# Kernel optimization log

Measured on AMD Instinct MI355X. Metric: run time of the kernel, lower is better.

Reference implementation:

```python
import jax, jax.numpy as jnp
import numpy as np

B, T, C = 2, 2048, 1024
H, HS = 16, 64
THETA = 10000.0


def _rope_tables(seq_len, dim, dtype):
    inv_freq = 1.0 / (THETA ** (jnp.arange(0, dim, 2, dtype=jnp.float32) / dim))
    t = jnp.arange(seq_len, dtype=jnp.float32)
    freqs = t[:, None] * inv_freq[None, :]          # [T, dim/2]
    emb = jnp.concatenate([freqs, freqs], axis=-1)  # [T, dim]
    return jnp.cos(emb).astype(dtype), jnp.sin(emb).astype(dtype)


def _rotate_half(x):
    x1, x2 = jnp.split(x, 2, axis=-1)
    return jnp.concatenate([-x2, x1], axis=-1)


def setup_inputs() -> dict:
    key = jax.random.key(0)
    ks = jax.random.split(key, 9)
    s = 0.02
    return {
        "q_x": jax.random.normal(ks[0], (B, T, C), dtype=jnp.float32),
        "wq": jax.random.normal(ks[1], (C, H * HS), dtype=jnp.float32) * s,
        "bq": jnp.zeros((H * HS,), dtype=jnp.float32),
        "wk": jax.random.normal(ks[2], (C, H * HS), dtype=jnp.float32) * s,
        "bk": jnp.zeros((H * HS,), dtype=jnp.float32),
        "wv": jax.random.normal(ks[3], (C, H * HS), dtype=jnp.float32) * s,
        "bv": jnp.zeros((H * HS,), dtype=jnp.float32),
        "wc": jax.random.normal(ks[4], (H * HS, C), dtype=jnp.float32) * s,
        "bc": jnp.zeros((C,), dtype=jnp.float32),
    }


def reference(q_x, wq, bq, wk, bk, wv, bv, wc, bc):
    b, t, _ = q_x.shape
    # Q/K/V projections -> [B, H, T, HS]
    q = (q_x @ wq + bq).reshape(b, t, H, HS).transpose(0, 2, 1, 3)
    k = (q_x @ wk + bk).reshape(b, t, H, HS).transpose(0, 2, 1, 3)
    v = (q_x @ wv + bv).reshape(b, t, H, HS).transpose(0, 2, 1, 3)
    # RoPE (concat-half rotation)
    cos, sin = _rope_tables(t, HS, q.dtype)  # [T, HS]
    q = q * cos + _rotate_half(q) * sin
    k = k * cos + _rotate_half(k) * sin
    # Naive causal attention
    scale = 1.0 / np.sqrt(HS)
    att = jnp.einsum("bhqd,bhkd->bhqk", q, k) * scale
    mask = jnp.tril(jnp.ones((t, t), dtype=bool))
    att = jnp.where(mask, att, -jnp.inf)
    att = jax.nn.softmax(att, axis=-1)
    y = jnp.einsum("bhqk,bhkd->bhqd", att, v)
    y = y.transpose(0, 2, 1, 3).reshape(b, t, H * HS)
    return y @ wc + bc
```

## Files before the change

### kernel.cpp

```cpp
#include <hip/hip_runtime.h>

#define B_  2
#define T_  2048
#define C_  1024
#define H_  16
#define HS_ 64
#define M_  4096
#define N_  1024
#define K_  1024

typedef float floatx4 __attribute__((ext_vector_type(4)));
typedef short bf16x8  __attribute__((ext_vector_type(8)));

__device__ __forceinline__ float bf2f(unsigned short u) {
    return __uint_as_float(((unsigned int)u) << 16);
}
__device__ __forceinline__ unsigned short f2bf(float f) {
    unsigned int u = __float_as_uint(f);
    return (unsigned short)((u + 0x7fffu + ((u >> 16) & 1u)) >> 16);
}
__device__ __forceinline__ unsigned int pack2(float a, float b) {
    return (unsigned int)f2bf(a) | ((unsigned int)f2bf(b) << 16);
}
__device__ __forceinline__ unsigned int pack2t(float a, float b) {
    return __builtin_amdgcn_perm(__float_as_uint(b), __float_as_uint(a), 0x07060302u);
}
__device__ __forceinline__ void async16(const unsigned short* g, unsigned short* l) {
    __builtin_amdgcn_global_load_lds(
        (const __attribute__((address_space(1))) unsigned int*)g,
        (__attribute__((address_space(3))) unsigned int*)l, 16, 0, 0);
}

__global__ __launch_bounds__(256) void prep_kernel(
    const float* __restrict__ x,
    const float* __restrict__ w0, const float* __restrict__ w1,
    const float* __restrict__ w2, const float* __restrict__ w3,
    unsigned short* __restrict__ xb, unsigned short* __restrict__ wTall)
{
    __shared__ float tile[64][65];
    const int bid = blockIdx.x;
    const int t = threadIdx.x;
    if (bid < 4096) {
        const size_t i = ((size_t)bid * 256 + t) * 4;
        const float4 v = *(const float4*)(x + i);
        ushort4 st;
        st.x = f2bf(v.x); st.y = f2bf(v.y); st.z = f2bf(v.z); st.w = f2bf(v.w);
        *(ushort4*)(xb + i) = st;
        return;
    }
    const int zb = bid - 4096;
    const int z = zb >> 8, rem = zb & 255;
    const float* w = (z == 0) ? w0 : (z == 1) ? w1 : (z == 2) ? w2 : w3;
    unsigned short* wT = wTall + ((size_t)z << 20);
    const int n0 = (rem & 15) * 64, k0 = (rem >> 4) * 64;

    const int r = t >> 2, cq = (t & 3) * 16;
    const float4* src = (const float4*)(w + (size_t)(k0 + r) * N_ + n0 + cq);
    const float4 v0 = src[0], v1 = src[1], v2 = src[2], v3 = src[3];
    tile[r][cq+0]=v0.x; tile[r][cq+1]=v0.y; tile[r][cq+2]=v0.z; tile[r][cq+3]=v0.w;
    tile[r][cq+4]=v1.x; tile[r][cq+5]=v1.y; tile[r][cq+6]=v1.z; tile[r][cq+7]=v1.w;
    tile[r][cq+8]=v2.x; tile[r][cq+9]=v2.y; tile[r][cq+10]=v2.z; tile[r][cq+11]=v2.w;
    tile[r][cq+12]=v3.x; tile[r][cq+13]=v3.y; tile[r][cq+14]=v3.z; tile[r][cq+15]=v3.w;
    __syncthreads();

    const int rn = t >> 2, ck = (t & 3) * 16;
    unsigned int o[8];
#pragma unroll
    for (int ii = 0; ii < 8; ii++)
        o[ii] = pack2(tile[ck + 2*ii][rn], tile[ck + 2*ii + 1][rn]);
    unsigned short* dst = wT + (size_t)(n0 + rn) * K_ + k0 + ck;
    *(uint4*)dst       = make_uint4(o[0], o[1], o[2], o[3]);
    *(uint4*)(dst + 8) = make_uint4(o[4], o[5], o[6], o[7]);
}

__global__ __launch_bounds__(512, 2) void qkv_gemm(
    const unsigned short* __restrict__ xb, const unsigned short* __restrict__ wT,
    const float* __restrict__ bq, const float* __restrict__ bk,
    const float* __restrict__ bv,
    unsigned short* __restrict__ qb, unsigned short* __restrict__ kb,
    unsigned short* __restrict__ vb)
{
    __shared__ unsigned short lds[65536];

    const int tid  = threadIdx.x;
    const int lane = tid & 63;
    const int wave = tid >> 6;

    const int bid = blockIdx.x;
    const int swz = (bid & 7) * 24 + (bid >> 3);
    const int nb  = swz % 12;
    const int mb  = swz / 12;
    const int m0  = mb * 256;
    const int n0g = nb * 256;

    const int wm = wave >> 2, wn = wave & 3;
    const int fr = lane & 15, quad = lane >> 4;

    const int r_s = tid >> 2;
    const int c_s = (tid & 3) ^ ((tid >> 3) & 3);
    const unsigned short* aS0 = xb + (size_t)(m0 + r_s) * 1024 + c_s * 8;
    const unsigned short* aS1 = aS0 + (size_t)128 * 1024;
    const unsigned short* bS0 = wT + (size_t)(n0g + r_s) * 1024 + c_s * 8;
    const unsigned short* bS1 = bS0 + (size_t)128 * 1024;
    unsigned short* ldw = &lds[wave * 512];

    auto stage = [&](int buf, int region, const unsigned short* s0,
                     const unsigned short* s1) {
        unsigned short* d = ldw + buf * 32768 + region * 8192;
        async16(s0, d);
        async16(s1, d + 4096);
    };

    int oA[8], oB[4];
#pragma unroll
    for (int i = 0; i < 8; i++) {
        const int r = wm * 128 + i * 16 + fr;
        oA[i] = r * 32 + ((quad ^ ((r >> 1) & 3)) << 3);
    }
#pragma unroll
    for (int j = 0; j < 4; j++) {
        const int r = wn * 64 + j * 16 + fr;
        oB[j] = r * 32 + ((quad ^ ((r >> 1) & 3)) << 3);
    }

    floatx4 acc[8][4];
#pragma unroll
    for (int i = 0; i < 8; i++)
#pragma unroll
        for (int j = 0; j < 4; j++) acc[i][j] = (floatx4){0.f, 0.f, 0.f, 0.f};

    stage(0, 0, aS0,      aS1);
    stage(0, 2, bS0,      bS1);
    stage(0, 1, aS0 + 32, aS1 + 32);
    stage(0, 3, bS0 + 32, bS1 + 32);
    stage(1, 0, aS0 + 64, aS1 + 64);
    stage(1, 2, bS0 + 64, bS1 + 64);
    asm volatile("s_waitcnt vmcnt(8)" ::: "memory");
    __builtin_amdgcn_s_barrier();
    __builtin_amdgcn_sched_barrier(0);

    bf16x8 af[4], bfr[4];
#pragma unroll 2
    for (int t = 0; t < 16; ++t) {
        const int cur = t & 1, nxt = cur ^ 1;
        const unsigned short* A0 = &lds[cur * 32768];
        const unsigned short* A1 = A0 + 8192;
        const unsigned short* B0 = A0 + 16384;
        const unsigned short* B1 = A0 + 24576;
        const int k1 = (t + 1) * 64, k2 = (t + 2) * 64;

#pragma unroll
        for (int i = 0; i < 4; i++) af[i]  = *(const bf16x8*)&A0[oA[i]];
#pragma unroll
        for (int j = 0; j < 4; j++) bfr[j] = *(const bf16x8*)&B0[oB[j]];
        if (t + 1 < 16) stage(nxt, 1, aS0 + k1 + 32, aS1 + k1 + 32);
        __builtin_amdgcn_s_barrier();
        asm volatile("s_waitcnt lgkmcnt(0)" ::: "memory");
        __builtin_amdgcn_s_setprio(1);
#pragma unroll
        for (int i = 0; i < 4; i++)
#pragma unroll
            for (int j = 0; j < 4; j++)
                acc[i][j] = __builtin_amdgcn_mfma_f32_16x16x32_bf16(
                    af[i], bfr[j], acc[i][j], 0, 0, 0);
        __builtin_amdgcn_s_setprio(0);
        __builtin_amdgcn_s_barrier();
        __builtin_amdgcn_sched_barrier(0);

#pragma unroll
        for (int i = 0; i < 4; i++) af[i] = *(const bf16x8*)&A0[oA[4 + i]];
        if (t + 1 < 16) stage(nxt, 3, bS0 + k1 + 32, bS1 + k1 + 32);
        asm volatile("s_waitcnt vmcnt(8)" ::: "memory");
        __builtin_amdgcn_s_barrier();
        asm volatile("s_waitcnt lgkmcnt(0)" ::: "memory");
        __builtin_amdgcn_s_setprio(1);
#pragma unroll
        for (int i = 0; i < 4; i++)
#pragma unroll
            for (int j = 0; j < 4; j++)
                acc[4 + i][j] = __builtin_amdgcn_mfma_f32_16x16x32_bf16(
                    af[i], bfr[j], acc[4 + i][j], 0, 0, 0);
        __builtin_amdgcn_s_setprio(0);
        __builtin_amdgcn_s_barrier();
        __builtin_amdgcn_sched_barrier(0);

#pragma unroll
        for (int i = 0; i < 4; i++) af[i]  = *(const bf16x8*)&A1[oA[i]];
#pragma unroll
        for (int j = 0; j < 4; j++) bfr[j] = *(const bf16x8*)&B1[oB[j]];
        if (t + 2 < 16) stage(cur, 0, aS0 + k2, aS1 + k2);
        __builtin_amdgcn_s_barrier();
        asm volatile("s_waitcnt lgkmcnt(0)" ::: "memory");
        __builtin_amdgcn_s_setprio(1);
#pragma unroll
        for (int i = 0; i < 4; i++)
#pragma unroll
            for (int j = 0; j < 4; j++)
                acc[i][j] = __builtin_amdgcn_mfma_f32_16x16x32_bf16(
                    af[i], bfr[j], acc[i][j], 0, 0, 0);
        __builtin_amdgcn_s_setprio(0);
        __builtin_amdgcn_s_barrier();
        __builtin_amdgcn_sched_barrier(0);

#pragma unroll
        for (int i = 0; i < 4; i++) af[i] = *(const bf16x8*)&A1[oA[4 + i]];
        if (t + 2 < 16) stage(cur, 2, bS0 + k2, bS1 + k2);
        asm volatile("s_waitcnt vmcnt(8)" ::: "memory");
        __builtin_amdgcn_s_barrier();
        asm volatile("s_waitcnt lgkmcnt(0)" ::: "memory");
        __builtin_amdgcn_s_setprio(1);
#pragma unroll
        for (int i = 0; i < 4; i++)
#pragma unroll
            for (int j = 0; j < 4; j++)
                acc[4 + i][j] = __builtin_amdgcn_mfma_f32_16x16x32_bf16(
                    af[i], bfr[j], acc[4 + i][j], 0, 0, 0);
        __builtin_amdgcn_s_setprio(0);
        __builtin_amdgcn_s_barrier();
        __builtin_amdgcn_sched_barrier(0);
    }

    const int p = nb >> 2;
    const int colbase = (nb & 3) * 256 + wn * 64;
    const int h = colbase >> 6;
    const int rb = quad * 4;
    const float* bias = (p == 0) ? bq : (p == 1) ? bk : bv;

    if (p == 2) {
#pragma unroll
        for (int j = 0; j < 4; j++) {
            const int d = j * 16 + fr;
            const float bz = bias[colbase + d];
#pragma unroll
            for (int i = 0; i < 8; i++) {
                const int row0 = m0 + wm * 128 + i * 16 + rb;
                const int bb = row0 >> 11, tt = row0 & 2047;
                ushort4 st;
                st.x = f2bf(acc[i][j][0] + bz);
                st.y = f2bf(acc[i][j][1] + bz);
                st.z = f2bf(acc[i][j][2] + bz);
                st.w = f2bf(acc[i][j][3] + bz);
                *(ushort4*)&vb[((size_t)(bb * H_ + h) * HS_ + d) * T_ + tt] = st;
            }
        }
    } else {
        unsigned short* out = (p == 0) ? qb : kb;
        const float qsc = (p == 0) ? 0.18033688011111772f : 1.0f;
        const float bz0 = bias[colbase + fr];
        const float bz1 = bias[colbase + 16 + fr];
        const float bz2 = bias[colbase + 32 + fr];
        const float bz3 = bias[colbase + 48 + fr];
        const float nl = -0.41524101186279297f;
        const float if0 = exp2f((float)fr * nl);
        const float if1 = exp2f((float)(fr + 16) * nl);
#pragma unroll
        for (int i = 0; i < 8; i++) {
#pragma unroll
            for (int pr = 0; pr < 4; pr++) {
                const int row = m0 + wm * 128 + i * 16 + rb + pr;
                const int bb = row >> 11, tt = row & 2047;
                float s0, c0, s1, c1;
                __sincosf((float)tt * if0, &s0, &c0);
                __sincosf((float)tt * if1, &s1, &c1);
                const float v0 = acc[i][0][pr] + bz0;
                const float v1 = acc[i][1][pr] + bz1;
                const float v2 = acc[i][2][pr] + bz2;
                const float v3 = acc[i][3][pr] + bz3;
                unsigned short* ob = out + ((size_t)(bb * H_ + h) * T_ + tt) * HS_ + fr;
                ob[0]  = f2bf((v0 * c0 - v2 * s0) * qsc);
                ob[16] = f2bf((v1 * c1 - v3 * s1) * qsc);
                ob[32] = f2bf((v2 * c0 + v0 * s0) * qsc);
                ob[48] = f2bf((v3 * c1 + v1 * s1) * qsc);
            }
        }
    }
}

__global__ __launch_bounds__(256) void attn_kernel(
    const unsigned short* __restrict__ qb, const unsigned short* __restrict__ kb,
    const unsigned short* __restrict__ vt, unsigned short* __restrict__ yb,
    unsigned short* __restrict__ Opart, float* __restrict__ Mpart)
{
    __shared__ unsigned short Ks[2][64 * 64];
    __shared__ unsigned short Vs[2][64 * 64];
    __shared__ unsigned short Ps[4][16 * 64];

    const int bh = blockIdx.x;
    const int b = bh >> 4, h = bh & 15;
    const int s = 47 - (int)blockIdx.y;
    int qt, ktlo, kthi, half;
    bool split;
    if (s < 16) { qt = s; ktlo = 0; kthi = qt; half = 0; split = false; }
    else {
        const int idx = s - 16;
        qt = 16 + (idx >> 1); half = idx & 1;
        const int nf = (qt + 2) >> 1;
        ktlo = half ? nf : 0;
        kthi = half ? qt : nf - 1;
        split = true;
    }
    const int r0 = qt * 64;
    const int tid  = threadIdx.x;
    const int lane = tid & 63;
    const int wave = tid >> 6;
    const int l4   = lane & 15;
    const int quad = lane >> 4;

    const int qrow_g = r0 + wave * 16 + l4;

    bf16x8 qf[2];
    {
        const unsigned short* qp = qb + ((size_t)bh * T_ + qrow_g) * HS_ + quad * 8;
        qf[0] = *(const bf16x8*)(qp);
        qf[1] = *(const bf16x8*)(qp + 32);
    }

    floatx4 o[4];
#pragma unroll
    for (int g = 0; g < 4; g++) o[g] = (floatx4){0.f, 0.f, 0.f, 0.f};
    float m = -1e30f, l = 0.f;

    const int srow = tid >> 2;
    const int sc16 = (tid & 3) * 16;
    const int ssw  = (srow & 7) * 8;
    const int psw  = (l4 & 7) * 8;

    const unsigned short* kp = kb + ((size_t)bh * T_ + srow) * HS_ + sc16;
    const unsigned short* vp = vt + ((size_t)(bh * 64 + srow)) * T_ + sc16;

    uint4 rk0 = *(const uint4*)(kp + (size_t)ktlo * 64 * HS_);
    uint4 rk1 = *(const uint4*)(kp + (size_t)ktlo * 64 * HS_ + 8);
    uint4 rv0 = *(const uint4*)(vp + ktlo * 64);
    uint4 rv1 = *(const uint4*)(vp + ktlo * 64 + 8);
    *(uint4*)&Ks[0][srow * 64 + ( sc16      ^ ssw)] = rk0;
    *(uint4*)&Ks[0][srow * 64 + ((sc16 + 8) ^ ssw)] = rk1;
    *(uint4*)&Vs[0][srow * 64 + ( sc16      ^ ssw)] = rv0;
    *(uint4*)&Vs[0][srow * 64 + ((sc16 + 8) ^ ssw)] = rv1;

    for (int kt = ktlo; kt <= kthi; kt++) {
        const int cur = (kt - ktlo) & 1;
        if (kt < kthi) {
            const unsigned short* kpn = kp + (size_t)(kt + 1) * (64 * HS_);
            const unsigned short* vpn = vp + (kt + 1) * 64;
            rk0 = *(const uint4*)kpn;
            rk1 = *(const uint4*)(kpn + 8);
            rv0 = *(const uint4*)vpn;
            rv1 = *(const uint4*)(vpn + 8);
        }
        __syncthreads();

        floatx4 sf[4];
        __builtin_amdgcn_s_setprio(1);
#pragma unroll
        for (int mg = 0; mg < 4; mg++) {
            const int key = mg * 16 + l4;
            const int ksw = (key & 7) * 8;
            const bf16x8 a0 = *(const bf16x8*)&Ks[cur][key * 64 + ( (quad * 8)       ^ ksw)];
            const bf16x8 a1 = *(const bf16x8*)&Ks[cur][key * 64 + (((quad * 8) + 32) ^ ksw)];
            floatx4 z = (floatx4){0.f, 0.f, 0.f, 0.f};
            z = __builtin_amdgcn_mfma_f32_16x16x32_bf16(a0, qf[0], z, 0, 0, 0);
            z = __builtin_amdgcn_mfma_f32_16x16x32_bf16(a1, qf[1], z, 0, 0, 0);
            sf[mg] = z;
        }
        __builtin_amdgcn_s_setprio(0);

        if (kt == qt) {
#pragma unroll
            for (int mg = 0; mg < 4; mg++)
#pragma unroll
                for (int r = 0; r < 4; r++)
                    if (kt * 64 + 16 * mg + quad * 4 + r > qrow_g)
                        sf[mg][r] = -1e30f;
        }

        float mx[4];
#pragma unroll
        for (int mg = 0; mg < 4; mg++)
            mx[mg] = fmaxf(fmaxf(sf[mg][0], sf[mg][1]),
                           fmaxf(sf[mg][2], sf[mg][3]));
        float tm = fmaxf(fmaxf(mx[0], mx[1]), fmaxf(mx[2], mx[3]));

        if (!__all(tm <= m + 8.f)) {
            tm = fmaxf(tm, __shfl_xor(tm, 16));
            tm = fmaxf(tm, __shfl_xor(tm, 32));
            const float mnew  = fmaxf(m, tm);
            const float alpha = __builtin_amdgcn_exp2f(m - mnew);
            l *= alpha;
#pragma unroll
            for (int g = 0; g < 4; g++) o[g] = o[g] * alpha;
            m = mnew;
        }

        float p[4][4];
        float psg[4];
#pragma unroll
        for (int mg = 0; mg < 4; mg++) {
#pragma unroll
            for (int r = 0; r < 4; r++)
                p[mg][r] = __builtin_amdgcn_exp2f(sf[mg][r] - m);
            psg[mg] = (p[mg][0] + p[mg][1]) + (p[mg][2] + p[mg][3]);
        }
        l += (psg[0] + psg[1]) + (psg[2] + psg[3]);

#pragma unroll
        for (int mg = 0; mg < 4; mg++) {
            const int kb4 = 16 * mg + quad * 4;
            const int off = ((kb4 & ~7) ^ psw) | (kb4 & 7);
            uint2 w;
            w.x = pack2t(p[mg][0], p[mg][1]);
            w.y = pack2t(p[mg][2], p[mg][3]);
            *(uint2*)&Ps[wave][l4 * 64 + off] = w;
        }

        const bf16x8 pf0 = *(const bf16x8*)&Ps[wave][l4 * 64 + ( (quad * 8)       ^ psw)];
        const bf16x8 pf1 = *(const bf16x8*)&Ps[wave][l4 * 64 + (((quad * 8) + 32) ^ psw)];
        __builtin_amdgcn_s_setprio(1);
#pragma unroll
        for (int g = 0; g < 4; g++) {
            const int vd  = g * 16 + l4;
            const int vsw = (vd & 7) * 8;
            const bf16x8 va0 = *(const bf16x8*)&Vs[cur][vd * 64 + ( (quad * 8)       ^ vsw)];
            const bf16x8 va1 = *(const bf16x8*)&Vs[cur][vd * 64 + (((quad * 8) + 32) ^ vsw)];
            o[g] = __builtin_amdgcn_mfma_f32_16x16x32_bf16(va0, pf0, o[g], 0, 0, 0);
            o[g] = __builtin_amdgcn_mfma_f32_16x16x32_bf16(va1, pf1, o[g], 0, 0, 0);
        }
        __builtin_amdgcn_s_setprio(0);

        if (kt < kthi) {
            const int nxt = cur ^ 1;
            *(uint4*)&Ks[nxt][srow * 64 + ( sc16      ^ ssw)] = rk0;
            *(uint4*)&Ks[nxt][srow * 64 + ((sc16 + 8) ^ ssw)] = rk1;
            *(uint4*)&Vs[nxt][srow * 64 + ( sc16      ^ ssw)] = rv0;
            *(uint4*)&Vs[nxt][srow * 64 + ((sc16 + 8) ^ ssw)] = rv1;
        }
    }

    l += __shfl_xor(l, 16);
    l += __shfl_xor(l, 32);

    if (!split) {
        const float invl = 1.f / l;
        unsigned short* yrow = yb + ((size_t)(b * T_ + qrow_g) * H_ + h) * HS_;
#pragma unroll
        for (int g = 0; g < 4; g++) {
            ushort4 st;
            st.x = f2bf(o[g][0] * invl);
            st.y = f2bf(o[g][1] * invl);
            st.z = f2bf(o[g][2] * invl);
            st.w = f2bf(o[g][3] * invl);
            *(ushort4*)&yrow[16 * g + quad * 4] = st;
        }
    } else {
        const int u  = (bh * 16 + (qt - 16)) * 2 + half;
        const int rl = wave * 16 + l4;
        unsigned short* Op = Opart + (size_t)u * 4096 + rl * 64;
#pragma unroll
        for (int g = 0; g < 4; g++) {
            ushort4 st;
            st.x = f2bf(o[g][0]);
            st.y = f2bf(o[g][1]);
            st.z = f2bf(o[g][2]);
            st.w = f2bf(o[g][3]);
            *(ushort4*)&Op[16 * g + quad * 4] = st;
        }
        if (quad == 0) {
            float* ml = Mpart + (size_t)u * 128;
            ml[rl]      = m;
            ml[64 + rl] = l;
        }
    }
}

__global__ __launch_bounds__(256) void attn_combine(
    const unsigned short* __restrict__ Opart, const float* __restrict__ Mpart,
    unsigned short* __restrict__ yb)
{
    const int u  = blockIdx.x;
    const int bh = u >> 4, qt = 16 + (u & 15);
    const int b = bh >> 4, h = bh & 15;
    const int t = threadIdx.x;
    const int r = t >> 2, c = (t & 3) * 16;

    const float* ml1 = Mpart + (size_t)(u * 2) * 128;
    const float* ml2 = ml1 + 128;
    const float m1 = ml1[r], l1 = ml1[64 + r];
    const float m2 = ml2[r], l2 = ml2[64 + r];
    const float M  = fmaxf(m1, m2);
    const float w1 = __builtin_amdgcn_exp2f(m1 - M);
    const float w2 = __builtin_amdgcn_exp2f(m2 - M);
    const float inv = 1.f / (l1 * w1 + l2 * w2);
    const float a1 = w1 * inv, a2 = w2 * inv;

    const unsigned short* O1 = Opart + (size_t)(u * 2)     * 4096 + r * 64 + c;
    const unsigned short* O2 = Opart + (size_t)(u * 2 + 1) * 4096 + r * 64 + c;
    unsigned short* yrow = yb + ((size_t)(b * T_ + qt * 64 + r) * H_ + h) * HS_ + c;

#pragma unroll
    for (int j = 0; j < 2; j++) {
        const uint4 u1 = *(const uint4*)(O1 + 8 * j);
        const uint4 u2 = *(const uint4*)(O2 + 8 * j);
        const unsigned int a[4] = {u1.x, u1.y, u1.z, u1.w};
        const unsigned int d[4] = {u2.x, u2.y, u2.z, u2.w};
        unsigned int ov[4];
#pragma unroll
        for (int q = 0; q < 4; q++) {
            const float y0 = bf2f((unsigned short)(a[q] & 0xffff)) * a1
                           + bf2f((unsigned short)(d[q] & 0xffff)) * a2;
            const float y1 = bf2f((unsigned short)(a[q] >> 16)) * a1
                           + bf2f((unsigned short)(d[q] >> 16)) * a2;
            ov[q] = pack2(y0, y1);
        }
        *(uint4*)(yrow + 8 * j) = make_uint4(ov[0], ov[1], ov[2], ov[3]);
    }
}

__global__ __launch_bounds__(256) void out_gemm(
    const unsigned short* __restrict__ A, const unsigned short* __restrict__ wcT,
    const float* __restrict__ bias, float* __restrict__ out)
{
    __shared__ unsigned short As[2 * 64 * 32];
    __shared__ unsigned short Bs[2 * 128 * 32];

    const int tid  = threadIdx.x;
    const int lane = tid & 63;
    const int wave = tid >> 6;
    const int n0 = blockIdx.x * 128;
    const int m0 = blockIdx.y * 64;

    const int lrow = lane >> 2, lch = (lane & 3) * 8;
    const unsigned short* ag  = A   + (size_t)(m0 + wave * 16 + lrow) * K_ + lch;
    const unsigned short* bg0 = wcT + (size_t)(n0 + wave * 32 + lrow) * K_ + lch;
    const unsigned short* bg1 = bg0 + (size_t)16 * K_;
    unsigned short* lA0  = &As[(wave * 16) * 32];
    unsigned short* lA1  = lA0 + 2048;
    unsigned short* lB00 = &Bs[(wave * 32) * 32];
    unsigned short* lB01 = &Bs[(wave * 32 + 16) * 32];
    unsigned short* lB10 = lB00 + 4096;
    unsigned short* lB11 = lB01 + 4096;

    const int fr = lane & 15;
    const int fk = (lane >> 4) * 8;
    const int wr2 = wave >> 1, wc2 = wave & 1;

    floatx4 acc[2][4];
#pragma unroll
    for (int i = 0; i < 2; i++)
#pragma unroll
        for (int j = 0; j < 4; j++) acc[i][j] = (floatx4){0.f, 0.f, 0.f, 0.f};

    for (int k0 = 0; k0 < K_; k0 += 64) {
        __syncthreads();
        async16(ag  + k0,      lA0);
        async16(ag  + k0 + 32, lA1);
        async16(bg0 + k0,      lB00);
        async16(bg1 + k0,      lB01);
        async16(bg0 + k0 + 32, lB10);
        async16(bg1 + k0 + 32, lB11);
        __syncthreads();

#pragma unroll
        for (int kh = 0; kh < 2; kh++) {
            const unsigned short* Ah = &As[kh * 2048];
            const unsigned short* Bh = &Bs[kh * 4096];
            bf16x8 af[2], bfr[4];
#pragma unroll
            for (int i = 0; i < 2; i++)
                af[i] = *(const bf16x8*)&Ah[(wr2 * 32 + i * 16 + fr) * 32 + fk];
#pragma unroll
            for (int j = 0; j < 4; j++)
                bfr[j] = *(const bf16x8*)&Bh[(wc2 * 64 + j * 16 + fr) * 32 + fk];
#pragma unroll
            for (int i = 0; i < 2; i++)
#pragma unroll
                for (int j = 0; j < 4; j++)
                    acc[i][j] = __builtin_amdgcn_mfma_f32_16x16x32_bf16(
                        af[i], bfr[j], acc[i][j], 0, 0, 0);
        }
    }

    const int rbase = (lane >> 4) * 4;
#pragma unroll
    for (int j = 0; j < 4; j++) {
        const int col = n0 + wc2 * 64 + j * 16 + fr;
        const float bz = bias[col];
#pragma unroll
        for (int i = 0; i < 2; i++) {
#pragma unroll
            for (int pr = 0; pr < 4; pr++) {
                const int row = m0 + wr2 * 32 + i * 16 + rbase + pr;
                out[(size_t)row * N_ + col] = acc[i][j][pr] + bz;
            }
        }
    }
}

extern "C" void kernel_launch(void* const* d_in, const int* in_sizes, int n_in,
                              void* d_out, int out_size, void* d_ws, size_t ws_size,
                              hipStream_t stream) {
    const float* x  = (const float*)d_in[0];
    const float* wq = (const float*)d_in[1];
    const float* bq = (const float*)d_in[2];
    const float* wk = (const float*)d_in[3];
    const float* bk = (const float*)d_in[4];
    const float* wv = (const float*)d_in[5];
    const float* bv = (const float*)d_in[6];
    const float* wc = (const float*)d_in[7];
    const float* bc = (const float*)d_in[8];
    float* out = (float*)d_out;

    unsigned short* ws  = (unsigned short*)d_ws;
    unsigned short* qb  = ws;
    unsigned short* kb  = ws + (size_t)4194304;
    unsigned short* vb  = ws + (size_t)8388608;
    unsigned short* yb  = ws + (size_t)12582912;
    unsigned short* xb  = ws + (size_t)16777216;
    unsigned short* wT  = ws + (size_t)20971520;
    unsigned short* wcT = wT + ((size_t)3 << 20);
    unsigned short* Opart = xb;
    float*          Mpart = (float*)wT;

    prep_kernel<<<5120, 256, 0, stream>>>(x, wq, wk, wv, wc, xb, wT);
    qkv_gemm<<<192, 512, 0, stream>>>(xb, wT, bq, bk, bv, qb, kb, vb);
    attn_kernel<<<dim3(32, 48), 256, 0, stream>>>(qb, kb, vb, yb, Opart, Mpart);
    attn_combine<<<512, 256, 0, stream>>>(Opart, Mpart, yb);
    out_gemm<<<dim3(8, 64), 256, 0, stream>>>(yb, wcT, bc, out);
}
```

Baseline: 188.6 us.

## Load K/V MFMA fragments directly from global memory, dropping LDS staging

The attention kernel no longer stages K and V tiles through double-buffered shared memory with a block-wide barrier. Each wave now loads its MFMA operand fragments straight from global memory (through L2/L1) every key tile, and launch bounds request four blocks per CU. This removes the LDS writes and reads and the per-tile __syncthreads, and less LDS per block may allow more resident blocks. In exchange, the four waves each fetch the same K/V data, which multiplies global/L2 traffic, and the register-staged prefetch of the next tile is gone, so load latency is exposed unless occupancy hides it.

```diff
diff --git a/kernel.cpp b/kernel.cpp
--- a/kernel.cpp
+++ b/kernel.cpp
@@ -276,13 +276,11 @@
     }
 }
 
-__global__ __launch_bounds__(256) void attn_kernel(
+__global__ __launch_bounds__(256, 4) void attn_kernel(
     const unsigned short* __restrict__ qb, const unsigned short* __restrict__ kb,
     const unsigned short* __restrict__ vt, unsigned short* __restrict__ yb,
     unsigned short* __restrict__ Opart, float* __restrict__ Mpart)
 {
-    __shared__ unsigned short Ks[2][64 * 64];
-    __shared__ unsigned short Vs[2][64 * 64];
     __shared__ unsigned short Ps[4][16 * 64];
 
     const int bh = blockIdx.x;
@@ -320,46 +318,27 @@
     for (int g = 0; g < 4; g++) o[g] = (floatx4){0.f, 0.f, 0.f, 0.f};
     float m = -1e30f, l = 0.f;
 
-    const int srow = tid >> 2;
-    const int sc16 = (tid & 3) * 16;
-    const int ssw  = (srow & 7) * 8;
-    const int psw  = (l4 & 7) * 8;
-
-    const unsigned short* kp = kb + ((size_t)bh * T_ + srow) * HS_ + sc16;
-    const unsigned short* vp = vt + ((size_t)(bh * 64 + srow)) * T_ + sc16;
-
-    uint4 rk0 = *(const uint4*)(kp + (size_t)ktlo * 64 * HS_);
-    uint4 rk1 = *(const uint4*)(kp + (size_t)ktlo * 64 * HS_ + 8);
-    uint4 rv0 = *(const uint4*)(vp + ktlo * 64);
-    uint4 rv1 = *(const uint4*)(vp + ktlo * 64 + 8);
-    *(uint4*)&Ks[0][srow * 64 + ( sc16      ^ ssw)] = rk0;
-    *(uint4*)&Ks[0][srow * 64 + ((sc16 + 8) ^ ssw)] = rk1;
-    *(uint4*)&Vs[0][srow * 64 + ( sc16      ^ ssw)] = rv0;
-    *(uint4*)&Vs[0][srow * 64 + ((sc16 + 8) ^ ssw)] = rv1;
+    const int psw = (l4 & 7) * 8;
+
+    const unsigned short* kfb = kb + ((size_t)bh * T_ + l4) * HS_ + quad * 8;
+    const unsigned short* vfb = vt + ((size_t)(bh * 64 + l4)) * T_ + quad * 8;
 
     for (int kt = ktlo; kt <= kthi; kt++) {
-        const int cur = (kt - ktlo) & 1;
-        if (kt < kthi) {
-            const unsigned short* kpn = kp + (size_t)(kt + 1) * (64 * HS_);
-            const unsigned short* vpn = vp + (kt + 1) * 64;
-            rk0 = *(const uint4*)kpn;
-            rk1 = *(const uint4*)(kpn + 8);
-            rv0 = *(const uint4*)vpn;
-            rv1 = *(const uint4*)(vpn + 8);
-        }
-        __syncthreads();
+        bf16x8 ka0[4], ka1[4];
+#pragma unroll
+        for (int mg = 0; mg < 4; mg++) {
+            const unsigned short* kr = kfb + (size_t)(kt * 64 + mg * 16) * HS_;
+            ka0[mg] = *(const bf16x8*)kr;
+            ka1[mg] = *(const bf16x8*)(kr + 32);
+        }
 
         floatx4 sf[4];
         __builtin_amdgcn_s_setprio(1);
 #pragma unroll
         for (int mg = 0; mg < 4; mg++) {
-            const int key = mg * 16 + l4;
-            const int ksw = (key & 7) * 8;
-            const bf16x8 a0 = *(const bf16x8*)&Ks[cur][key * 64 + ( (quad * 8)       ^ ksw)];
-            const bf16x8 a1 = *(const bf16x8*)&Ks[cur][key * 64 + (((quad * 8) + 32) ^ ksw)];
             floatx4 z = (floatx4){0.f, 0.f, 0.f, 0.f};
-            z = __builtin_amdgcn_mfma_f32_16x16x32_bf16(a0, qf[0], z, 0, 0, 0);
-            z = __builtin_amdgcn_mfma_f32_16x16x32_bf16(a1, qf[1], z, 0, 0, 0);
+            z = __builtin_amdgcn_mfma_f32_16x16x32_bf16(ka0[mg], qf[0], z, 0, 0, 0);
+            z = __builtin_amdgcn_mfma_f32_16x16x32_bf16(ka1[mg], qf[1], z, 0, 0, 0);
             sf[mg] = z;
         }
         __builtin_amdgcn_s_setprio(0);
@@ -412,27 +391,23 @@
             *(uint2*)&Ps[wave][l4 * 64 + off] = w;
         }
 
+        bf16x8 va0[4], va1[4];
+#pragma unroll
+        for (int g = 0; g < 4; g++) {
+            const unsigned short* vr = vfb + (size_t)(g * 16) * T_ + kt * 64;
+            va0[g] = *(const bf16x8*)vr;
+            va1[g] = *(const bf16x8*)(vr + 32);
+        }
+
         const bf16x8 pf0 = *(const bf16x8*)&Ps[wave][l4 * 64 + ( (quad * 8)       ^ psw)];
         const bf16x8 pf1 = *(const bf16x8*)&Ps[wave][l4 * 64 + (((quad * 8) + 32) ^ psw)];
         __builtin_amdgcn_s_setprio(1);
 #pragma unroll
         for (int g = 0; g < 4; g++) {
-            const int vd  = g * 16 + l4;
-            const int vsw = (vd & 7) * 8;
-            const bf16x8 va0 = *(const bf16x8*)&Vs[cur][vd * 64 + ( (quad * 8)       ^ vsw)];
-            const bf16x8 va1 = *(const bf16x8*)&Vs[cur][vd * 64 + (((quad * 8) + 32) ^ vsw)];
-            o[g] = __builtin_amdgcn_mfma_f32_16x16x32_bf16(va0, pf0, o[g], 0, 0, 0);
-            o[g] = __builtin_amdgcn_mfma_f32_16x16x32_bf16(va1, pf1, o[g], 0, 0, 0);
+            o[g] = __builtin_amdgcn_mfma_f32_16x16x32_bf16(va0[g], pf0, o[g], 0, 0, 0);
+            o[g] = __builtin_amdgcn_mfma_f32_16x16x32_bf16(va1[g], pf1, o[g], 0, 0, 0);
         }
         __builtin_amdgcn_s_setprio(0);
-
-        if (kt < kthi) {
-            const int nxt = cur ^ 1;
-            *(uint4*)&Ks[nxt][srow * 64 + ( sc16      ^ ssw)] = rk0;
-            *(uint4*)&Ks[nxt][srow * 64 + ((sc16 + 8) ^ ssw)] = rk1;
-            *(uint4*)&Vs[nxt][srow * 64 + ( sc16      ^ ssw)] = rv0;
-            *(uint4*)&Vs[nxt][srow * 64 + ((sc16 + 8) ^ ssw)] = rv1;
-        }
     }
 
     l += __shfl_xor(l, 16);
```

Result: slower. 293.2 us (+55.4%).

## Rewrite output GEMM with 128x128 tiles, swizzled LDS, and async double-buffered pipeline

Applied to the files above, without the earlier changes.

Replaces the simple synchronous out_gemm (64x128 tiles, syncthreads per K-step) with a version modeled on the qkv_gemm: 128x128 tiles, XOR-swizzled LDS layout, async global-to-LDS staging double-buffered across K-steps with split waitcnt/barrier phases and setprio around MFMA bursts, plus block index swizzling for L2 locality. It also makes the vmcnt waits in both GEMMs drain fully on the last iterations, so the tail no longer relies on a fixed outstanding-load count. The aim is to hide global load latency behind MFMA work and cut the number of barriers per FLOP. The price is fewer blocks (256) and higher register use.

```diff
diff --git a/kernel.cpp b/kernel.cpp
--- a/kernel.cpp
+++ b/kernel.cpp
@@ -170,7 +170,8 @@
 #pragma unroll
         for (int i = 0; i < 4; i++) af[i] = *(const bf16x8*)&A0[oA[4 + i]];
         if (t + 1 < 16) stage(nxt, 3, bS0 + k1 + 32, bS1 + k1 + 32);
-        asm volatile("s_waitcnt vmcnt(8)" ::: "memory");
+        if (t < 15) { asm volatile("s_waitcnt vmcnt(8)" ::: "memory"); }
+        else        { asm volatile("s_waitcnt vmcnt(0)" ::: "memory"); }
         __builtin_amdgcn_s_barrier();
         asm volatile("s_waitcnt lgkmcnt(0)" ::: "memory");
         __builtin_amdgcn_s_setprio(1);
@@ -205,7 +206,8 @@
 #pragma unroll
         for (int i = 0; i < 4; i++) af[i] = *(const bf16x8*)&A1[oA[4 + i]];
         if (t + 2 < 16) stage(cur, 2, bS0 + k2, bS1 + k2);
-        asm volatile("s_waitcnt vmcnt(8)" ::: "memory");
+        if (t < 14) { asm volatile("s_waitcnt vmcnt(8)" ::: "memory"); }
+        else        { asm volatile("s_waitcnt vmcnt(0)" ::: "memory"); }
         __builtin_amdgcn_s_barrier();
         asm volatile("s_waitcnt lgkmcnt(0)" ::: "memory");
         __builtin_amdgcn_s_setprio(1);
@@ -514,80 +516,162 @@
     }
 }
 
-__global__ __launch_bounds__(256) void out_gemm(
+__global__ __launch_bounds__(256, 2) void out_gemm(
     const unsigned short* __restrict__ A, const unsigned short* __restrict__ wcT,
     const float* __restrict__ bias, float* __restrict__ out)
 {
-    __shared__ unsigned short As[2 * 64 * 32];
-    __shared__ unsigned short Bs[2 * 128 * 32];
+    __shared__ unsigned short lds[32768];
 
     const int tid  = threadIdx.x;
     const int lane = tid & 63;
     const int wave = tid >> 6;
-    const int n0 = blockIdx.x * 128;
-    const int m0 = blockIdx.y * 64;
-
-    const int lrow = lane >> 2, lch = (lane & 3) * 8;
-    const unsigned short* ag  = A   + (size_t)(m0 + wave * 16 + lrow) * K_ + lch;
-    const unsigned short* bg0 = wcT + (size_t)(n0 + wave * 32 + lrow) * K_ + lch;
-    const unsigned short* bg1 = bg0 + (size_t)16 * K_;
-    unsigned short* lA0  = &As[(wave * 16) * 32];
-    unsigned short* lA1  = lA0 + 2048;
-    unsigned short* lB00 = &Bs[(wave * 32) * 32];
-    unsigned short* lB01 = &Bs[(wave * 32 + 16) * 32];
-    unsigned short* lB10 = lB00 + 4096;
-    unsigned short* lB11 = lB01 + 4096;
-
-    const int fr = lane & 15;
-    const int fk = (lane >> 4) * 8;
-    const int wr2 = wave >> 1, wc2 = wave & 1;
-
-    floatx4 acc[2][4];
-#pragma unroll
-    for (int i = 0; i < 2; i++)
+
+    const int bid = blockIdx.x;
+    const int swz = (bid & 7) * 32 + (bid >> 3);
+    const int nt  = swz >> 5;
+    const int mt  = swz & 31;
+    const int m0  = mt * 128;
+    const int n0  = nt * 128;
+
+    const int wm = wave >> 1, wn = wave & 1;
+    const int fr = lane & 15, quad = lane >> 4;
+
+    const int r_s = tid >> 2;
+    const int c_s = (tid & 3) ^ ((tid >> 3) & 3);
+    const unsigned short* aS0 = A   + (size_t)(m0 + r_s) * 1024 + c_s * 8;
+    const unsigned short* aS1 = aS0 + (size_t)64 * 1024;
+    const unsigned short* bS0 = wcT + (size_t)(n0 + r_s) * 1024 + c_s * 8;
+    const unsigned short* bS1 = bS0 + (size_t)64 * 1024;
+    unsigned short* ldw = &lds[wave * 512];
+
+    auto stage = [&](int buf, int region, const unsigned short* s0,
+                     const unsigned short* s1) {
+        unsigned short* d = ldw + buf * 16384 + region * 4096;
+        async16(s0, d);
+        async16(s1, d + 2048);
+    };
+
+    int oA[4], oB[4];
+#pragma unroll
+    for (int i = 0; i < 4; i++) {
+        const int r = wm * 64 + i * 16 + fr;
+        oA[i] = r * 32 + ((quad ^ ((r >> 1) & 3)) << 3);
+    }
+#pragma unroll
+    for (int j = 0; j < 4; j++) {
+        const int r = wn * 64 + j * 16 + fr;
+        oB[j] = r * 32 + ((quad ^ ((r >> 1) & 3)) << 3);
+    }
+
+    floatx4 acc[4][4];
+#pragma unroll
+    for (int i = 0; i < 4; i++)
 #pragma unroll
         for (int j = 0; j < 4; j++) acc[i][j] = (floatx4){0.f, 0.f, 0.f, 0.f};
 
-    for (int k0 = 0; k0 < K_; k0 += 64) {
-        __syncthreads();
-        async16(ag  + k0,      lA0);
-        async16(ag  + k0 + 32, lA1);
-        async16(bg0 + k0,      lB00);
-        async16(bg1 + k0,      lB01);
-        async16(bg0 + k0 + 32, lB10);
-        async16(bg1 + k0 + 32, lB11);
-        __syncthreads();
-
-#pragma unroll
-        for (int kh = 0; kh < 2; kh++) {
-            const unsigned short* Ah = &As[kh * 2048];
-            const unsigned short* Bh = &Bs[kh * 4096];
-            bf16x8 af[2], bfr[4];
-#pragma unroll
-            for (int i = 0; i < 2; i++)
-                af[i] = *(const bf16x8*)&Ah[(wr2 * 32 + i * 16 + fr) * 32 + fk];
+    stage(0, 0, aS0,      aS1);
+    stage(0, 2, bS0,      bS1);
+    stage(0, 1, aS0 + 32, aS1 + 32);
+    stage(0, 3, bS0 + 32, bS1 + 32);
+    stage(1, 0, aS0 + 64, aS1 + 64);
+    stage(1, 2, bS0 + 64, bS1 + 64);
+    asm volatile("s_waitcnt vmcnt(8)" ::: "memory");
+    __builtin_amdgcn_s_barrier();
+    __builtin_amdgcn_sched_barrier(0);
+
+    bf16x8 af[2], bfr[4];
+#pragma unroll 2
+    for (int t = 0; t < 16; ++t) {
+        const int cur = t & 1, nxt = cur ^ 1;
+        const unsigned short* A0 = &lds[cur * 16384];
+        const unsigned short* A1 = A0 + 4096;
+        const unsigned short* B0 = A0 + 8192;
+        const unsigned short* B1 = A0 + 12288;
+        const int k1 = (t + 1) * 64, k2 = (t + 2) * 64;
+
+#pragma unroll
+        for (int i = 0; i < 2; i++) af[i]  = *(const bf16x8*)&A0[oA[i]];
+#pragma unroll
+        for (int j = 0; j < 4; j++) bfr[j] = *(const bf16x8*)&B0[oB[j]];
+        if (t + 1 < 16) stage(nxt, 1, aS0 + k1 + 32, aS1 + k1 + 32);
+        __builtin_amdgcn_s_barrier();
+        asm volatile("s_waitcnt lgkmcnt(0)" ::: "memory");
+        __builtin_amdgcn_s_setprio(1);
+#pragma unroll
+        for (int i = 0; i < 2; i++)
 #pragma unroll
             for (int j = 0; j < 4; j++)
-                bfr[j] = *(const bf16x8*)&Bh[(wc2 * 64 + j * 16 + fr) * 32 + fk];
-#pragma unroll
-            for (int i = 0; i < 2; i++)
-#pragma unroll
-                for (int j = 0; j < 4; j++)
-                    acc[i][j] = __builtin_amdgcn_mfma_f32_16x16x32_bf16(
-                        af[i], bfr[j], acc[i][j], 0, 0, 0);
-        }
-    }
-
-    const int rbase = (lane >> 4) * 4;
+                acc[i][j] = __builtin_amdgcn_mfma_f32_16x16x32_bf16(
+                    af[i], bfr[j], acc[i][j], 0, 0, 0);
+        __builtin_amdgcn_s_setprio(0);
+        __builtin_amdgcn_s_barrier();
+        __builtin_amdgcn_sched_barrier(0);
+
+#pragma unroll
+        for (int i = 0; i < 2; i++) af[i] = *(const bf16x8*)&A0[oA[2 + i]];
+        if (t + 1 < 16) stage(nxt, 3, bS0 + k1 + 32, bS1 + k1 + 32);
+        if (t < 15) { asm volatile("s_waitcnt vmcnt(8)" ::: "memory"); }
+        else        { asm volatile("s_waitcnt vmcnt(0)" ::: "memory"); }
+        __builtin_amdgcn_s_barrier();
+        asm volatile("s_waitcnt lgkmcnt(0)" ::: "memory");
+        __builtin_amdgcn_s_setprio(1);
+#pragma unroll
+        for (int i = 0; i < 2; i++)
+#pragma unroll
+            for (int j = 0; j < 4; j++)
+                acc[2 + i][j] = __builtin_amdgcn_mfma_f32_16x16x32_bf16(
+                    af[i], bfr[j], acc[2 + i][j], 0, 0, 0);
+        __builtin_amdgcn_s_setprio(0);
+        __builtin_amdgcn_s_barrier();
+        __builtin_amdgcn_sched_barrier(0);
+
+#pragma unroll
+        for (int i = 0; i < 2; i++) af[i]  = *(const bf16x8*)&A1[oA[i]];
+#pragma unroll
+        for (int j = 0; j < 4; j++) bfr[j] = *(const bf16x8*)&B1[oB[j]];
+        if (t + 2 < 16) stage(cur, 0, aS0 + k2, aS1 + k2);
+        __builtin_amdgcn_s_barrier();
+        asm volatile("s_waitcnt lgkmcnt(0)" ::: "memory");
+        __builtin_amdgcn_s_setprio(1);
+#pragma unroll
+        for (int i = 0; i < 2; i++)
+#pragma unroll
+            for (int j = 0; j < 4; j++)
+                acc[i][j] = __builtin_amdgcn_mfma_f32_16x16x32_bf16(
+                    af[i], bfr[j], acc[i][j], 0, 0, 0);
+        __builtin_amdgcn_s_setprio(0);
+        __builtin_amdgcn_s_barrier();
+        __builtin_amdgcn_sched_barrier(0);
+
+#pragma unroll
+        for (int i = 0; i < 2; i++) af[i] = *(const bf16x8*)&A1[oA[2 + i]];
+        if (t + 2 < 16) stage(cur, 2, bS0 + k2, bS1 + k2);
+        if (t < 14) { asm volatile("s_waitcnt vmcnt(8)" ::: "memory"); }
+        else        { asm volatile("s_waitcnt vmcnt(0)" ::: "memory"); }
+        __builtin_amdgcn_s_barrier();
+        asm volatile("s_waitcnt lgkmcnt(0)" ::: "memory");
+        __builtin_amdgcn_s_setprio(1);
+#pragma unroll
+        for (int i = 0; i < 2; i++)
+#pragma unroll
+            for (int j = 0; j < 4; j++)
+                acc[2 + i][j] = __builtin_amdgcn_mfma_f32_16x16x32_bf16(
+                    af[i], bfr[j], acc[2 + i][j], 0, 0, 0);
+        __builtin_amdgcn_s_setprio(0);
+        __builtin_amdgcn_s_barrier();
+        __builtin_amdgcn_sched_barrier(0);
+    }
+
+    const int rbase = quad * 4;
 #pragma unroll
     for (int j = 0; j < 4; j++) {
-        const int col = n0 + wc2 * 64 + j * 16 + fr;
+        const int col = n0 + wn * 64 + j * 16 + fr;
         const float bz = bias[col];
 #pragma unroll
-        for (int i = 0; i < 2; i++) {
+        for (int i = 0; i < 4; i++) {
 #pragma unroll
             for (int pr = 0; pr < 4; pr++) {
-                const int row = m0 + wr2 * 32 + i * 16 + rbase + pr;
+                const int row = m0 + wm * 64 + i * 16 + rbase + pr;
                 out[(size_t)row * N_ + col] = acc[i][j][pr] + bz;
             }
         }
@@ -623,5 +707,5 @@
     qkv_gemm<<<192, 512, 0, stream>>>(xb, wT, bq, bk, bv, qb, kb, vb);
     attn_kernel<<<dim3(32, 48), 256, 0, stream>>>(qb, kb, vb, yb, Opart, Mpart);
     attn_combine<<<512, 256, 0, stream>>>(Opart, Mpart, yb);
-    out_gemm<<<dim3(8, 64), 256, 0, stream>>>(yb, wcT, bc, out);
-}
+    out_gemm<<<256, 256, 0, stream>>>(yb, wcT, bc, out);
+}
```

Measured after the change: 188.0 us. No clear change (-0.3%).
